# Kernel optimization log

Measured on AMD Instinct MI355X. Metric: run time of the kernel, lower is better.

## Reference

```python
import jax, jax.numpy as jnp
import numpy as np

HEAD_NUM = 16

def setup_inputs() -> dict:
    key = jax.random.key(0)
    k1, k2 = jax.random.split(key)
    bs, seq, d = 2, 2048, 1024
    embeddings = jax.random.normal(k1, (bs, seq, d), dtype=jnp.float32)
    W = jax.random.normal(k2, (d, 3 * d), dtype=jnp.float32) * (1.0 / np.sqrt(d))
    b = jnp.zeros((3 * d,), dtype=jnp.float32)
    return {"embeddings": embeddings, "W": W, "b": b}

def reference(embeddings, W, b):
    bs, seq, d = embeddings.shape
    h = HEAD_NUM
    qkv = embeddings @ W + b                      # [b, s, 3d]
    q, k, v = jnp.split(qkv, 3, axis=-1)          # each [b, s, d]
    hd = d // h
    # Faithful to source: reshape to (bs, seq, head_dim, heads) then permute
    def split_heads(x, head_dim):
        return x.reshape(bs, seq, head_dim, h).transpose(0, 3, 1, 2)  # [b, h, s, hd]
    mq = split_heads(q, hd)
    mk = split_heads(k, hd)
    mv = split_heads(v, hd)
    scale = jnp.sqrt(jnp.asarray(hd, dtype=mq.dtype))
    scores = jnp.einsum('bhqd,bhkd->bhqk', mq, mk) / scale  # [b, h, s, s]
    attn = jax.nn.softmax(scores, axis=-1)
    out = jnp.einsum('bhqk,bhkv->bhqv', attn, mv)            # [b, h, s, hd]
    return out.transpose(0, 2, 1, 3).reshape(bs, seq, -1)    # [b, s, d]
```

## Files before the change

### kernel.cpp

```cpp
#include <hip/hip_runtime.h>
#include <stdint.h>

typedef unsigned short u16;
typedef unsigned int u32;
typedef unsigned int u32x2 __attribute__((ext_vector_type(2)));
typedef float f32x4 __attribute__((ext_vector_type(4)));
typedef __bf16 bf16x8 __attribute__((ext_vector_type(8)));

#define BS 2
#define SEQ 2048
#define DIM 1024
#define NW3 3072
#define NH 16
#define HD 64

#define MFMA_BF16(a, b, c) __builtin_amdgcn_mfma_f32_16x16x32_bf16((a), (b), (c), 0, 0, 0)

#define GLL16(g, l)                                                                \
  __builtin_amdgcn_global_load_lds(                                                \
      (__attribute__((address_space(1))) void*)(void*)(uintptr_t)(g),              \
      (__attribute__((address_space(3))) void*)(l), 16, 0, 0)

__device__ __forceinline__ float fexp2(float x) {
#if defined(__has_builtin)
#if __has_builtin(__builtin_amdgcn_exp2f)
  return __builtin_amdgcn_exp2f(x);
#else
  return exp2f(x);
#endif
#else
  return exp2f(x);
#endif
}

__device__ __forceinline__ u16 f2bf(float x) {
  __bf16 h = (__bf16)x;
  return __builtin_bit_cast(u16, h);
}

#define CSC 0.18033688011112042f

#if defined(__has_builtin)
#if __has_builtin(__builtin_amdgcn_permlane32_swap) && \
    __has_builtin(__builtin_amdgcn_permlane16_swap)
#define HAVE_PLSWAP 1
#endif
#endif

__device__ __forceinline__ uint4 p_transform(u32 pk00, u32 pk01, u32 pk10, u32 pk11,
                                             int sl0, int sl1, bool hi) {
#ifdef HAVE_PLSWAP
  u32x2 s0 = __builtin_amdgcn_permlane32_swap(pk00, pk10, false, false);
  u32x2 s1 = __builtin_amdgcn_permlane32_swap(pk01, pk11, false, false);
  u32x2 t0 = __builtin_amdgcn_permlane16_swap(s0[0], s0[1], false, false);
  u32x2 t1 = __builtin_amdgcn_permlane16_swap(s1[0], s1[1], false, false);
  uint4 wv;
  wv.x = t0[0]; wv.y = t1[0]; wv.z = t0[1]; wv.w = t1[1];
  return wv;
#else
  u32 a0 = __shfl(pk00, sl0), a1 = __shfl(pk01, sl0);
  u32 a2 = __shfl(pk00, sl1), a3 = __shfl(pk01, sl1);
  u32 b0 = __shfl(pk10, sl0), b1 = __shfl(pk11, sl0);
  u32 b2 = __shfl(pk10, sl1), b3 = __shfl(pk11, sl1);
  uint4 wv;
  wv.x = hi ? b0 : a0; wv.y = hi ? b1 : a1;
  wv.z = hi ? b2 : a2; wv.w = hi ? b3 : a3;
  return wv;
#endif
}

__global__ __launch_bounds__(256) void conv_kernel(const float* __restrict__ A,
                                                   u16* __restrict__ O,
                                                   const float* __restrict__ W,
                                                   u16* __restrict__ Wt) {
  if (blockIdx.x < 4096) {
    int i = (blockIdx.x * 256 + threadIdx.x) * 4;
    float4 v = *(const float4*)(A + i);
    union { u16 u[4]; ushort4 v4; } p;
    p.u[0] = f2bf(v.x); p.u[1] = f2bf(v.y); p.u[2] = f2bf(v.z); p.u[3] = f2bf(v.w);
    *(ushort4*)(O + i) = p.v4;
  } else {
    int id = (blockIdx.x - 4096) * 256 + threadIdx.x;
    int kc = id / NW3;
    int n = id - kc * NW3;
    union { u16 u[8]; uint4 v; } p;
#pragma unroll
    for (int i = 0; i < 8; ++i) p.u[i] = f2bf(W[(kc * 8 + i) * NW3 + n]);
    int h = n & 15, hd = (n & 1023) >> 4;
    int np = (n & ~1023) + h * 64 + hd;
    *(uint4*)(Wt + np * DIM + kc * 8) = p.v;
  }
}

#define GSTAGE(ADST, BDST, KT)                                                 \
  {                                                                            \
    const int koff = (KT) * 64;                                \
    _Pragma("unroll") for (int r = 0; r < 2; ++r) {                            \
      int l = r * 256 + t;                            \
      int row = l >> 2, pos = l & 3;                                           \
      int kc = pos ^ (row & 3);                                                \
      GLL16(Abase + row * 2048 + koff + kc * 16, (char*)(ADST) + l * 16);      \
      GLL16(Bbase + row * 2048 + koff + kc * 16, (char*)(BDST) + l * 16);      \
    }                                                                          \
  }

#define GCOMPUTE(AT, BT)                                                       \
  {                                                                            \
    bf16x8 af[4], bfr[4];                                                      \
    _Pragma("unroll") for (int mt = 0; mt < 4; ++mt) {                         \
      int row = wm + mt * 16 + c;                                              \
      int kc = quad ^ (row & 3);                                               \
      af[mt] = *(const bf16x8*)((const char*)(AT) + row * 64 + kc * 16);       \
    }                                                                          \
    _Pragma("unroll") for (int nt = 0; nt < 4; ++nt) {                         \
      int row = wn + nt * 16 + c;                                              \
      int kc = quad ^ (row & 3);                                               \
      bfr[nt] = *(const bf16x8*)((const char*)(BT) + row * 64 + kc * 16);      \
    }                                                                          \
    _Pragma("unroll") for (int mt = 0; mt < 4; ++mt)                           \
      _Pragma("unroll") for (int nt = 0; nt < 4; ++nt)                         \
        acc[mt][nt] = MFMA_BF16(af[mt], bfr[nt], acc[mt][nt]);                 \
  }

__global__ __launch_bounds__(256) void gemm_qkv_kernel(
    const u16* __restrict__ Ab, const u16* __restrict__ Bt, const float* __restrict__ bias,
    u16* __restrict__ Q, u16* __restrict__ K, u16* __restrict__ Vt) {
  __shared__ __align__(16) u16 Aa[128 * 32];
  __shared__ __align__(16) u16 Ab2[128 * 32];
  __shared__ __align__(16) u16 Ba[128 * 32];
  __shared__ __align__(16) u16 Bb2[128 * 32];
  const int t = threadIdx.x;
  const int lane = t & 63, wave = t >> 6;
  const int c = lane & 15, quad = lane >> 4;
  const int tm = blockIdx.x / 24, tn = blockIdx.x - tm * 24;
  const int wm = (wave >> 1) * 64, wn = (wave & 1) * 64;

  const char* Abase = (const char*)(Ab + (size_t)tm * 128 * DIM);
  const char* Bbase = (const char*)(Bt + (size_t)tn * 128 * DIM);

  f32x4 z = {0.f, 0.f, 0.f, 0.f};
  f32x4 acc[4][4];
#pragma unroll
  for (int i = 0; i < 4; ++i)
#pragma unroll
    for (int j = 0; j < 4; ++j) acc[i][j] = z;

  GSTAGE(Aa, Ba, 0);
  __syncthreads();
  for (int kt = 0; kt < 32; kt += 2) {
    GSTAGE(Ab2, Bb2, kt + 1);
    GCOMPUTE(Aa, Ba);
    __syncthreads();
    if (kt + 2 < 32) GSTAGE(Aa, Ba, kt + 2);
    GCOMPUTE(Ab2, Bb2);
    __syncthreads();
  }

#pragma unroll
  for (int nt = 0; nt < 4; ++nt) {
    int np = tn * 128 + wn + nt * 16 + c;
    int which = np >> 10;
    int rem = np & 1023;
    int h = rem >> 6, hd = rem & 63;
    float bv = bias[(np & ~1023) + hd * 16 + h];
    float sc = (which == 0) ? CSC : 1.0f;
    float bvs = bv * sc;
#pragma unroll
    for (int mt = 0; mt < 4; ++mt) {
      int mbase = tm * 128 + wm + mt * 16 + quad * 4;
      int bI = mbase >> 11;
      int s0 = mbase & 2047;
      if (which == 2) {
        union { u16 u[4]; uint2 v; } p;
#pragma unroll
        for (int r = 0; r < 4; ++r) p.u[r] = f2bf(acc[mt][nt][r] + bv);
        *(uint2*)(Vt + ((size_t)(bI * NH + h) * HD + hd) * SEQ + s0) = p.v;
      } else {
        u16* dst = (which == 0) ? Q : K;
#pragma unroll
        for (int r = 0; r < 4; ++r)
          dst[((size_t)(bI * NH + h) * SEQ + (s0 + r)) * HD + hd] =
              f2bf(acc[mt][nt][r] * sc + bvs);
      }
    }
  }
}

#define STAGE_KV(KDST, VDST, KTILE)                                            \
  {                                                                            \
    const char* Ktb = Kb + (size_t)(KTILE) * 8192;        \
    const char* Vtb = Vb + (size_t)(KTILE) * 128;         \
    _Pragma("unroll") for (int r = 0; r < 2; ++r) {                            \
      int l = r * 256 + t;                                                     \
      int row = l >> 3, pos = l & 7;                                           \
      int kc = pos ^ (row & 7);                                                \
      GLL16(Ktb + row * 128 + kc * 16, (char*)(KDST) + l * 16);                \
      GLL16(Vtb + row * 4096 + kc * 16, (char*)(VDST) + l * 16);               \
    }                                                                          \
  }

#define COMPUTE_TILE(KT, VT)                                                   \
  {                                                                            \
    f32x4 sT[2][2]; \
    sT[0][0] = z; sT[0][1] = z; sT[1][0] = z; sT[1][1] = z;                    \
    __builtin_amdgcn_s_setprio(1);                                             \
    _Pragma("unroll") for (int mt2 = 0; mt2 < 2; ++mt2) {                      \
      _Pragma("unroll") for (int ks = 0; ks < 2; ++ks) {                       \
        int row = ws * 32 + mt2 * 16 + c;                                      \
        int kc = (ks * 4 + quad) ^ (row & 7);                                  \
        bf16x8 kf = *(const bf16x8*)((const char*)(KT) + row * 128 + kc * 16); \
        sT[mt2][0] = MFMA_BF16(kf, qf[0][ks], sT[mt2][0]);                     \
        sT[mt2][1] = MFMA_BF16(kf, qf[1][ks], sT[mt2][1]);                     \
      }                                                                        \
    }                                                                          \
    __builtin_amdgcn_s_setprio(0);                                             \
    bf16x8 pf[2];                                                              \
    _Pragma("unroll") for (int nt = 0; nt < 2; ++nt) {                         \
      u32 pk[2][2];                                                            \
      _Pragma("unroll") for (int mt2 = 0; mt2 < 2; ++mt2) {                    \
        float p0 = fexp2(sT[mt2][nt][0]);                                      \
        float p1 = fexp2(sT[mt2][nt][1]);                                      \
        float p2 = fexp2(sT[mt2][nt][2]);                                      \
        float p3 = fexp2(sT[mt2][nt][3]);                                      \
        smA[nt] += p0 + p1; smB[nt] += p2 + p3;                                \
        pk[mt2][0] = (u32)f2bf(p0) | ((u32)f2bf(p1) << 16);                    \
        pk[mt2][1] = (u32)f2bf(p2) | ((u32)f2bf(p3) << 16);                    \
      }                                                                        \
      uint4 wv = p_transform(pk[0][0], pk[0][1], pk[1][0], pk[1][1],           \
                             sl0, sl1, hi);                                    \
      pf[nt] = __builtin_bit_cast(bf16x8, wv);                                 \
    }                                                                          \
    __builtin_amdgcn_s_setprio(1);                                             \
    _Pragma("unroll") for (int mt = 0; mt < 4; ++mt) {                         \
      int row = mt * 16 + c;                                                   \
      int kc = vq ^ (row & 7);                                                 \
      bf16x8 vf = *(const bf16x8*)((const char*)(VT) + row * 128 + kc * 16);   \
      accO[mt][0] = MFMA_BF16(vf, pf[0], accO[mt][0]);                         \
      accO[mt][1] = MFMA_BF16(vf, pf[1], accO[mt][1]);                         \
    }                                                                          \
    __builtin_amdgcn_s_setprio(0);                                             \
  }

__global__ __launch_bounds__(256, 4) void attn_kernel(
    const u16* __restrict__ Q, const u16* __restrict__ K,
    const u16* __restrict__ Vt, float* __restrict__ Out) {
  __shared__ __align__(16) u16 Ka[64 * 64];
  __shared__ __align__(16) u16 Kb2[64 * 64];
  __shared__ __align__(16) u16 Va[64 * 64];
  __shared__ __align__(16) u16 Vb2[64 * 64];
  const int t = threadIdx.x;
  const int lane = t & 63, wave = t >> 6;
  const int c = lane & 15, quad = lane >> 4;
  const int wq = wave & 1, ws = wave >> 1;
  const int p = blockIdx.x;
  const int xcd = p & 7, slot = p >> 3;
  const int bh = xcd + ((slot >> 5) << 3);
  const int qt = slot & 31;
  const int h = bh & 15, b = bh >> 4;

  const u16* Qb = Q + ((size_t)bh * SEQ + qt * 64) * HD;
  const char* Kb = (const char*)(K + (size_t)bh * SEQ * HD);
  const char* Vb = (const char*)(Vt + (size_t)bh * HD * SEQ);

#pragma unroll
  for (int r = 0; r < 2; ++r) {
    int l = r * 256 + t;
    int row = l >> 3, pos = l & 7;
    int kc = pos ^ (row & 7);
    GLL16((const char*)Qb + row * 128 + kc * 16, (char*)Ka + l * 16);
  }
  __syncthreads();
  bf16x8 qf[2][2];
#pragma unroll
  for (int nt = 0; nt < 2; ++nt)
#pragma unroll
    for (int ks = 0; ks < 2; ++ks) {
      int row = wq * 32 + nt * 16 + c;
      int kc = (ks * 4 + quad) ^ (row & 7);
      qf[nt][ks] = *(const bf16x8*)((const char*)Ka + row * 128 + kc * 16);
    }
  __syncthreads();

  float smA[2] = {0.f, 0.f}, smB[2] = {0.f, 0.f};
  f32x4 z = {0.f, 0.f, 0.f, 0.f};
  f32x4 accO[4][2];
#pragma unroll
  for (int i = 0; i < 4; ++i) { accO[i][0] = z; accO[i][1] = z; }

  const int sl0 = c + 16 * ((quad & 1) * 2);
  const int sl1 = sl0 + 16;
  const bool hi = quad >= 2;
  const int vq = ws * 4 + quad;

  STAGE_KV(Ka, Va, 0);
  __syncthreads();

  for (int kt = 0; kt < 32; kt += 2) {
    STAGE_KV(Kb2, Vb2, kt + 1);
    COMPUTE_TILE(Ka, Va);
    __syncthreads();
    if (kt + 2 < 32) STAGE_KV(Ka, Va, kt + 2);
    COMPUTE_TILE(Kb2, Vb2);
    __syncthreads();
  }

  float sm[2];
#pragma unroll
  for (int nt = 0; nt < 2; ++nt) {
    float s = smA[nt] + smB[nt];
    s += __shfl_xor(s, 16);
    s += __shfl_xor(s, 32);
    sm[nt] = s;
  }
  if (ws == 1) {
    float* fb = (float*)(wq ? (void*)Kb2 : (void*)Ka);
#pragma unroll
    for (int mt = 0; mt < 4; ++mt)
#pragma unroll
      for (int nt = 0; nt < 2; ++nt)
        *(f32x4*)(fb + (mt * 2 + nt) * 256 + lane * 4) = accO[mt][nt];
    float* lb = (float*)Va + wq * 128;
    lb[lane * 2] = sm[0];
    lb[lane * 2 + 1] = sm[1];
  }
  __syncthreads();
  if (ws == 0) {
    const float* fb = (const float*)(wq ? (void*)Kb2 : (void*)Ka);
#pragma unroll
    for (int mt = 0; mt < 4; ++mt)
#pragma unroll
      for (int nt = 0; nt < 2; ++nt)
        accO[mt][nt] += *(const f32x4*)(fb + (mt * 2 + nt) * 256 + lane * 4);
    const float* lb = (const float*)Va + wq * 128;
    float inv0 = 1.f / (sm[0] + lb[lane * 2]);
    float inv1 = 1.f / (sm[1] + lb[lane * 2 + 1]);
    int s0 = qt * 64 + wq * 32 + c;
#pragma unroll
    for (int mt = 0; mt < 4; ++mt) {
#pragma unroll
      for (int nt = 0; nt < 2; ++nt) {
        float inv = nt ? inv1 : inv0;
        float4 o;
        o.x = accO[mt][nt][0] * inv;
        o.y = accO[mt][nt][1] * inv;
        o.z = accO[mt][nt][2] * inv;
        o.w = accO[mt][nt][3] * inv;
        size_t off = ((size_t)(b * SEQ + s0 + nt * 16)) * DIM + h * HD + mt * 16 + quad * 4;
        *(float4*)(Out + off) = o;
      }
    }
  }
}

extern "C" void kernel_launch(void* const* d_in, const int* in_sizes, int n_in,
                              void* d_out, int out_size, void* d_ws, size_t ws_size,
                              hipStream_t stream) {
  (void)in_sizes; (void)n_in; (void)out_size; (void)ws_size;
  const float* emb = (const float*)d_in[0];
  const float* W = (const float*)d_in[1];
  const float* bias = (const float*)d_in[2];
  float* out = (float*)d_out;
  char* ws = (char*)d_ws;
  u16* Ab = (u16*)ws;
  u16* Wt = (u16*)(ws + 8388608);
  u16* Qd = (u16*)(ws + 14680064);
  u16* Kd = (u16*)(ws + 23068672);
  u16* Vd = (u16*)(ws + 31457280);

  conv_kernel<<<5632, 256, 0, stream>>>(emb, Ab, W, Wt);
  gemm_qkv_kernel<<<768, 256, 0, stream>>>(Ab, Wt, bias, Qd, Kd, Vd);
  attn_kernel<<<1024, 256, 0, stream>>>(Qd, Kd, Vd, out);
}
```

Before: 164.8 us.

## Tile weight transpose through LDS and compute softmax row sums via MFMA

The weight conversion now reads 64x64 tiles with coalesced float4 loads, transposes them through shared memory and writes 16 contiguous bf16 values per thread. This replaces strided scalar global reads and cuts the block count. In the attention kernel, the softmax denominator is accumulated by an extra MFMA against a ones vector instead of per-element scalar adds and cross-lane shuffles. This moves VALU work onto the matrix unit at the cost of two extra MFMAs per tile. The LDS tile reads in the transpose step may hit bank conflicts.

```diff
diff --git a/kernel.cpp b/kernel.cpp
--- a/kernel.cpp
+++ b/kernel.cpp
@@ -80,15 +80,30 @@
     p.u[0] = f2bf(v.x); p.u[1] = f2bf(v.y); p.u[2] = f2bf(v.z); p.u[3] = f2bf(v.w);
     *(ushort4*)(O + i) = p.v4;
   } else {
-    int id = (blockIdx.x - 4096) * 256 + threadIdx.x;
-    int kc = id / NW3;
-    int n = id - kc * NW3;
-    union { u16 u[8]; uint4 v; } p;
-#pragma unroll
-    for (int i = 0; i < 8; ++i) p.u[i] = f2bf(W[(kc * 8 + i) * NW3 + n]);
+    __shared__ __align__(16) u16 lt[64][68];
+    int b2 = blockIdx.x - 4096;
+    int ktile = b2 / 48, ntile = b2 - ktile * 48;
+    int k0 = ktile * 64, n0 = ntile * 64;
+    int rowb = threadIdx.x >> 4, c4 = (threadIdx.x & 15) * 4;
+#pragma unroll
+    for (int rr = 0; rr < 4; ++rr) {
+      int row = rowb + rr * 16;
+      float4 v = *(const float4*)(W + (size_t)(k0 + row) * NW3 + n0 + c4);
+      union { u16 u[4]; uint2 d; } pk;
+      pk.u[0] = f2bf(v.x); pk.u[1] = f2bf(v.y); pk.u[2] = f2bf(v.z); pk.u[3] = f2bf(v.w);
+      *(uint2*)&lt[row][c4] = pk.d;
+    }
+    __syncthreads();
+    int j = threadIdx.x >> 2, seg = threadIdx.x & 3;
+    int n = n0 + j;
     int h = n & 15, hd = (n & 1023) >> 4;
     int np = (n & ~1023) + h * 64 + hd;
-    *(uint4*)(Wt + np * DIM + kc * 8) = p.v;
+    union { u16 u[16]; uint4 q[2]; } o;
+#pragma unroll
+    for (int idx = 0; idx < 16; ++idx) o.u[idx] = lt[seg * 16 + idx][j];
+    u16* dst = Wt + (size_t)np * DIM + k0 + seg * 16;
+    *(uint4*)(dst) = o.q[0];
+    *(uint4*)(dst + 8) = o.q[1];
   }
 }
 
@@ -222,7 +237,6 @@
         float p1 = fexp2(sT[mt2][nt][1]);                                      \
         float p2 = fexp2(sT[mt2][nt][2]);                                      \
         float p3 = fexp2(sT[mt2][nt][3]);                                      \
-        smA[nt] += p0 + p1; smB[nt] += p2 + p3;                                \
         pk[mt2][0] = (u32)f2bf(p0) | ((u32)f2bf(p1) << 16);                    \
         pk[mt2][1] = (u32)f2bf(p2) | ((u32)f2bf(p3) << 16);                    \
       }                                                                        \
@@ -238,6 +252,8 @@
       accO[mt][0] = MFMA_BF16(vf, pf[0], accO[mt][0]);                         \
       accO[mt][1] = MFMA_BF16(vf, pf[1], accO[mt][1]);                         \
     }                                                                          \
+    acc_l[0] = MFMA_BF16(ones, pf[0], acc_l[0]);   \
+    acc_l[1] = MFMA_BF16(ones, pf[1], acc_l[1]);                               \
     __builtin_amdgcn_s_setprio(0);                                             \
   }
 
@@ -281,11 +297,13 @@
     }
   __syncthreads();
 
-  float smA[2] = {0.f, 0.f}, smB[2] = {0.f, 0.f};
   f32x4 z = {0.f, 0.f, 0.f, 0.f};
   f32x4 accO[4][2];
 #pragma unroll
   for (int i = 0; i < 4; ++i) { accO[i][0] = z; accO[i][1] = z; }
+  f32x4 acc_l[2] = {z, z};
+  const uint4 onesw = {0x3F803F80u, 0x3F803F80u, 0x3F803F80u, 0x3F803F80u};
+  const bf16x8 ones = __builtin_bit_cast(bf16x8, onesw);
 
   const int sl0 = c + 16 * ((quad & 1) * 2);
   const int sl1 = sl0 + 16;
@@ -305,13 +323,8 @@
   }
 
   float sm[2];
-#pragma unroll
-  for (int nt = 0; nt < 2; ++nt) {
-    float s = smA[nt] + smB[nt];
-    s += __shfl_xor(s, 16);
-    s += __shfl_xor(s, 32);
-    sm[nt] = s;
-  }
+  sm[0] = acc_l[0][0];
+  sm[1] = acc_l[1][0];
   if (ws == 1) {
     float* fb = (float*)(wq ? (void*)Kb2 : (void*)Ka);
 #pragma unroll
@@ -367,7 +380,7 @@
   u16* Kd = (u16*)(ws + 23068672);
   u16* Vd = (u16*)(ws + 31457280);
 
-  conv_kernel<<<5632, 256, 0, stream>>>(emb, Ab, W, Wt);
+  conv_kernel<<<4864, 256, 0, stream>>>(emb, Ab, W, Wt);
   gemm_qkv_kernel<<<768, 256, 0, stream>>>(Ab, Wt, bias, Qd, Kd, Vd);
   attn_kernel<<<1024, 256, 0, stream>>>(Qd, Kd, Vd, out);
 }
```

Result: no change. 162.6 us (-1.3%).
